# Performance work log

Measured on AMD Instinct MI355X. Metric: run time of the kernel, lower is better.

## Reference

```python
import jax, jax.numpy as jnp
import numpy as np

P, Q, R = 6, 0, 0
N = P + Q + R
DIM = 1 << N  # 64 basis blades


def _cayley_table(p, q, r):
    """Dense [dim, dim, dim] Cayley tensor C with C[a, b, a^b] = sign(a, b).
    Basis blades are indexed by bitmasks; sign combines the canonical
    reordering parity with the metric signature (+1 x p, -1 x q, 0 x r)."""
    n = p + q + r
    dim = 1 << n
    metric = [1.0] * p + [-1.0] * q + [0.0] * r
    C = np.zeros((dim, dim, dim), dtype=np.float32)
    for a in range(dim):
        for b in range(dim):
            # reorder parity: count transpositions to sort blade product
            s = 1.0
            aa = a >> 1
            cnt = 0
            while aa:
                cnt += bin(aa & b).count('1')
                aa >>= 1
            if cnt & 1:
                s = -s
            # metric contribution from repeated basis vectors
            for i in range(n):
                if (a >> i) & 1 and (b >> i) & 1:
                    s *= metric[i]
            C[a, b, a ^ b] = s
    return C

CAYLEY = jnp.asarray(_cayley_table(P, Q, R))  # [64, 64, 64], highly sparse


def setup_inputs() -> dict:
    key = jax.random.key(0)
    kx, kw = jax.random.split(key)
    x = jax.random.normal(kx, (1048576, DIM), dtype=jnp.float32)
    weight = jax.random.normal(kw, (DIM,), dtype=jnp.float32)
    return {"x": x, "weight": weight}


def reference(x, weight):
    # geometric_product(x, weight) with weight broadcast over the batch:
    # out[b, k] = sum_{i,j} C[i, j, k] * x[b, i] * weight[j]
    # Contract C with the shared weight first (tiny [dim, dim] matrix),
    # then apply to every batch element.
    M = jnp.einsum('ijk,j->ik', CAYLEY, weight)  # [64, 64]
    return x @ M  # [B, 64]
```

## Files before the change

### kernel.cpp

```cpp
#include <hip/hip_runtime.h>
#include <hip/hip_bf16.h>


#define DIM 64
#define TPB 256
#define ROWS 256

typedef __attribute__((ext_vector_type(8))) short  bf16x8;
typedef __attribute__((ext_vector_type(4))) float  f32x4;

__device__ __forceinline__ unsigned short f2bf(float v) {
    __hip_bfloat16 hb = __float2bfloat16(v);
    return *reinterpret_cast<unsigned short*>(&hb);
}

__global__ void build_Mt(const float* __restrict__ w, unsigned short* __restrict__ Mt) {
    int t = threadIdx.x + blockIdx.x * blockDim.x;
    if (t >= 8 * 64 * 8) return;
    int f  = t >> 9;
    int kc = f >> 2, ab = f & 3;
    int rem = t & 511;
    int l = rem >> 3, e = rem & 7;
    int k = kc * 32 + ((l >> 4) << 3) + e;
    int a = (ab << 4) + (l & 15);
    int j = k ^ a;
    int aa = k >> 1, cnt = 0;
    while (aa) { cnt += __popc(aa & j); aa >>= 1; }
    float v = (cnt & 1) ? -w[j] : w[j];
    Mt[t] = f2bf(v);
}

__global__ __launch_bounds__(TPB, 4)
void gp_main_kernel(const float* __restrict__ x,
                    const unsigned short* __restrict__ Mt,
                    float* __restrict__ out) {
    const int tid  = threadIdx.x;
    const int lane = tid & 63;
    const int wv   = tid >> 6;
    const int r15  = lane & 15;
    const int g    = lane >> 4;

    bf16x8 af[2][4];
    const bf16x8* __restrict__ Mtv = (const bf16x8*)Mt;
    #pragma unroll
    for (int kc = 0; kc < 2; ++kc)
        #pragma unroll
        for (int ab = 0; ab < 4; ++ab)
            af[kc][ab] = Mtv[(kc * 4 + ab) * 64 + lane];

    const long long rowbase = (long long)blockIdx.x * ROWS + (long long)wv * 64;

    float4 raw[4][4];
    #pragma unroll
    for (int bb = 0; bb < 4; ++bb) {
        const float4* __restrict__ p =
            (const float4*)(x + (rowbase + bb * 16 + r15) * DIM) + g * 2;
        raw[bb][0] = p[0];
        raw[bb][1] = p[1];
        raw[bb][2] = p[8];
        raw[bb][3] = p[9];
    }

    float4* __restrict__ outp = (float4*)out;

    #pragma unroll
    for (int bb = 0; bb < 4; ++bb) {
        bf16x8 bfr[2];
        #pragma unroll
        for (int kc = 0; kc < 2; ++kc) {
            const float* s = (const float*)&raw[bb][kc * 2];
            bf16x8 t;
            #pragma unroll
            for (int e = 0; e < 8; ++e) t[e] = (short)f2bf(s[e]);
            bfr[kc] = t;
        }

        f32x4 acc[4];
        #pragma unroll
        for (int ab = 0; ab < 4; ++ab) acc[ab] = (f32x4){0.f, 0.f, 0.f, 0.f};
        #pragma unroll
        for (int kc = 0; kc < 2; ++kc)
            #pragma unroll
            for (int ab = 0; ab < 4; ++ab)
                acc[ab] = __builtin_amdgcn_mfma_f32_16x16x32_bf16(
                    af[kc][ab], bfr[kc], acc[ab], 0, 0, 0);

        const long long rg = rowbase + bb * 16 + r15;
        #pragma unroll
        for (int ab = 0; ab < 4; ++ab)
            outp[rg * 16 + ab * 4 + g] =
                make_float4(acc[ab][0], acc[ab][1], acc[ab][2], acc[ab][3]);
    }
}

extern "C" void kernel_launch(void* const* d_in, const int* in_sizes, int n_in,
                              void* d_out, int out_size, void* d_ws, size_t ws_size,
                              hipStream_t stream) {
    const float* x = (const float*)d_in[0];
    const float* w = (const float*)d_in[1];
    float* out = (float*)d_out;
    unsigned short* Mt = (unsigned short*)d_ws;

    int nrows = in_sizes[0] / DIM;
    int nblocks = nrows / ROWS;

    build_Mt<<<16, 256, 0, stream>>>(w, Mt);
    gp_main_kernel<<<nblocks, TPB, 0, stream>>>(x, Mt, out);
}
```

Measured before the change: 123.1 us.

## Stage x tile through LDS via direct global-to-LDS loads with XOR swizzle

The kernel now loads the x tile with async global_load_lds into a swizzled shared buffer, so each wave's global reads are fully coalesced instead of strided per-lane float4 reads. Rows per block drop from 256 to 64 and launch bounds rise to 8 blocks/SM, so each wave handles one 16-row MFMA tile. This adds a __syncthreads and an LDS round trip, and launches four times as many blocks.

```diff
diff --git a/kernel.cpp b/kernel.cpp
--- a/kernel.cpp
+++ b/kernel.cpp
@@ -4,10 +4,13 @@
 
 #define DIM 64
 #define TPB 256
-#define ROWS 256
+#define ROWS 64
 
 typedef __attribute__((ext_vector_type(8))) short  bf16x8;
 typedef __attribute__((ext_vector_type(4))) float  f32x4;
+
+typedef const unsigned int __attribute__((address_space(1)))* gu32p;
+typedef unsigned int __attribute__((address_space(3)))* su32p;
 
 __device__ __forceinline__ unsigned short f2bf(float v) {
     __hip_bfloat16 hb = __float2bfloat16(v);
@@ -30,15 +33,31 @@
     Mt[t] = f2bf(v);
 }
 
-__global__ __launch_bounds__(TPB, 4)
+__global__ __launch_bounds__(TPB, 8)
 void gp_main_kernel(const float* __restrict__ x,
                     const unsigned short* __restrict__ Mt,
                     float* __restrict__ out) {
+    __shared__ float xs[ROWS * DIM];
+
     const int tid  = threadIdx.x;
     const int lane = tid & 63;
     const int wv   = tid >> 6;
     const int r15  = lane & 15;
     const int g    = lane >> 4;
+
+    const long long rowbase = (long long)blockIdx.x * ROWS;
+    const float4* __restrict__ xin = (const float4*)x;
+
+    #pragma unroll
+    for (int it = 0; it < 4; ++it) {
+        int idx  = it * TPB + tid;
+        int row  = idx >> 4;
+        int f4   = idx & 15;
+        int c    = ((f4 >> 1) ^ (row & 7));
+        long long src = (rowbase + row) * 16 + c * 2 + (f4 & 1);
+        __builtin_amdgcn_global_load_lds((gu32p)(xin + src),
+                                         (su32p)&xs[idx * 4], 16, 0, 0);
+    }
 
     bf16x8 af[2][4];
     const bf16x8* __restrict__ Mtv = (const bf16x8*)Mt;
@@ -48,49 +67,40 @@
         for (int ab = 0; ab < 4; ++ab)
             af[kc][ab] = Mtv[(kc * 4 + ab) * 64 + lane];
 
-    const long long rowbase = (long long)blockIdx.x * ROWS + (long long)wv * 64;
+    __syncthreads();
 
-    float4 raw[4][4];
+    const int r_loc = wv * 16 + r15;
+    bf16x8 bfr[2];
     #pragma unroll
-    for (int bb = 0; bb < 4; ++bb) {
-        const float4* __restrict__ p =
-            (const float4*)(x + (rowbase + bb * 16 + r15) * DIM) + g * 2;
-        raw[bb][0] = p[0];
-        raw[bb][1] = p[1];
-        raw[bb][2] = p[8];
-        raw[bb][3] = p[9];
+    for (int kc = 0; kc < 2; ++kc) {
+        int s = (kc * 4 + g) ^ (r_loc & 7);
+        const float* src = &xs[r_loc * DIM + s * 8];
+        float4 lo = *reinterpret_cast<const float4*>(src);
+        float4 hi = *reinterpret_cast<const float4*>(src + 4);
+        bf16x8 t;
+        t[0] = (short)f2bf(lo.x); t[1] = (short)f2bf(lo.y);
+        t[2] = (short)f2bf(lo.z); t[3] = (short)f2bf(lo.w);
+        t[4] = (short)f2bf(hi.x); t[5] = (short)f2bf(hi.y);
+        t[6] = (short)f2bf(hi.z); t[7] = (short)f2bf(hi.w);
+        bfr[kc] = t;
     }
 
-    float4* __restrict__ outp = (float4*)out;
-
+    f32x4 acc[4];
     #pragma unroll
-    for (int bb = 0; bb < 4; ++bb) {
-        bf16x8 bfr[2];
-        #pragma unroll
-        for (int kc = 0; kc < 2; ++kc) {
-            const float* s = (const float*)&raw[bb][kc * 2];
-            bf16x8 t;
-            #pragma unroll
-            for (int e = 0; e < 8; ++e) t[e] = (short)f2bf(s[e]);
-            bfr[kc] = t;
-        }
-
-        f32x4 acc[4];
-        #pragma unroll
-        for (int ab = 0; ab < 4; ++ab) acc[ab] = (f32x4){0.f, 0.f, 0.f, 0.f};
-        #pragma unroll
-        for (int kc = 0; kc < 2; ++kc)
-            #pragma unroll
-            for (int ab = 0; ab < 4; ++ab)
-                acc[ab] = __builtin_amdgcn_mfma_f32_16x16x32_bf16(
-                    af[kc][ab], bfr[kc], acc[ab], 0, 0, 0);
-
-        const long long rg = rowbase + bb * 16 + r15;
+    for (int ab = 0; ab < 4; ++ab) acc[ab] = (f32x4){0.f, 0.f, 0.f, 0.f};
+    #pragma unroll
+    for (int kc = 0; kc < 2; ++kc)
         #pragma unroll
         for (int ab = 0; ab < 4; ++ab)
-            outp[rg * 16 + ab * 4 + g] =
-                make_float4(acc[ab][0], acc[ab][1], acc[ab][2], acc[ab][3]);
-    }
+            acc[ab] = __builtin_amdgcn_mfma_f32_16x16x32_bf16(
+                af[kc][ab], bfr[kc], acc[ab], 0, 0, 0);
+
+    float4* __restrict__ outp = (float4*)out;
+    const long long rg = rowbase + r_loc;
+    #pragma unroll
+    for (int ab = 0; ab < 4; ++ab)
+        outp[rg * 16 + ab * 4 + g] =
+            make_float4(acc[ab][0], acc[ab][1], acc[ab][2], acc[ab][3]);
 }
 
 extern "C" void kernel_launch(void* const* d_in, const int* in_sizes, int n_in,
```

Result: faster. 103.0 us, median of 2 (-16.3%).
